# Optimization experiments

Hardware: AMD Instinct MI355X
Metric: run time of the kernel (lower is better)

Reference implementation:

```python
import jax, jax.numpy as jnp
import numpy as np

NT, NP = 100000, 20000
FT, FP, H = 128, 64, 128
E, EL = 2000000, 500000
EPS = 1e-12


def _l2norm(x):
    # F.normalize(x, p=2, dim=-1): x / max(||x||, eps)
    n = jnp.sqrt(jnp.sum(x * x, axis=-1, keepdims=True))
    return x / jnp.maximum(n, EPS)


def _seg_mean(x_src, src_idx, dst_idx, n_dst, inv_cnt):
    # gather src features per edge, scatter-sum to dst, divide by in-degree
    s = jax.ops.segment_sum(x_src[src_idx], dst_idx, num_segments=n_dst)
    return s * inv_cnt[:, None]


def setup_inputs() -> dict:
    key = jax.random.key(0)
    ks = jax.random.split(key, 24)

    def w(k, fan_in, fan_out):
        return jax.random.normal(k, (fan_in, fan_out), jnp.float32) / np.sqrt(fan_in)

    inp = {
        "x_track": jax.random.normal(ks[0], (NT, FT), jnp.float32),
        "x_playlist": jax.random.normal(ks[1], (NP, FP), jnp.float32),
        "edge_src": jax.random.randint(ks[2], (E,), 0, NT),
        "edge_dst": jax.random.randint(ks[3], (E,), 0, NP),
        "label_src": jax.random.randint(ks[4], (EL,), 0, NT),
        "label_dst": jax.random.randint(ks[5], (EL,), 0, NP),
        # per-type input projections (PyG Linear, bias=True)
        "Wn_t": w(ks[6], FT, H), "bn_t": jnp.zeros((H,), jnp.float32),
        "Wn_p": w(ks[7], FP, H), "bn_p": jnp.zeros((H,), jnp.float32),
        # layer1: edge type track->playlist (dst playlist) and reverse (dst track)
        "W1_l_p": w(ks[8], H, H), "b1_p": jnp.zeros((H,), jnp.float32), "W1_r_p": w(ks[9], H, H),
        "W1_l_t": w(ks[10], H, H), "b1_t": jnp.zeros((H,), jnp.float32), "W1_r_t": w(ks[11], H, H),
        # layer2
        "W2_l_p": w(ks[12], H, H), "b2_p": jnp.zeros((H,), jnp.float32), "W2_r_p": w(ks[13], H, H),
        "W2_l_t": w(ks[14], H, H), "b2_t": jnp.zeros((H,), jnp.float32), "W2_r_t": w(ks[15], H, H),
    }
    return inp


def reference(x_track, x_playlist, edge_src, edge_dst, label_src, label_dst,
              Wn_t, bn_t, Wn_p, bn_p,
              W1_l_p, b1_p, W1_r_p, W1_l_t, b1_t, W1_r_t,
              W2_l_p, b2_p, W2_r_p, W2_l_t, b2_t, W2_r_t):
    nt, np_ = x_track.shape[0], x_playlist.shape[0]
    ones = jnp.ones(edge_src.shape, jnp.float32)
    inv_cnt_p = 1.0 / jnp.maximum(jax.ops.segment_sum(ones, edge_dst, num_segments=np_), 1.0)
    inv_cnt_t = 1.0 / jnp.maximum(jax.ops.segment_sum(ones, edge_src, num_segments=nt), 1.0)

    # per-type input linear
    h_t = x_track @ Wn_t + bn_t        # [NT, H]
    h_p = x_playlist @ Wn_p + bn_p     # [NP, H]

    # hetero SAGE layer 1 (normalize=True) + relu
    agg_p = _seg_mean(h_t, edge_src, edge_dst, np_, inv_cnt_p)  # track -> playlist
    agg_t = _seg_mean(h_p, edge_dst, edge_src, nt, inv_cnt_t)   # playlist -> track (rev edges)
    o_p = jax.nn.relu(_l2norm(agg_p @ W1_l_p + b1_p + h_p @ W1_r_p))
    o_t = jax.nn.relu(_l2norm(agg_t @ W1_l_t + b1_t + h_t @ W1_r_t))

    # hetero SAGE layer 2 (normalize=True), no relu
    agg_p2 = _seg_mean(o_t, edge_src, edge_dst, np_, inv_cnt_p)
    agg_t2 = _seg_mean(o_p, edge_dst, edge_src, nt, inv_cnt_t)
    z_p = _l2norm(agg_p2 @ W2_l_p + b2_p + o_p @ W2_r_p)
    z_t = _l2norm(agg_t2 @ W2_l_t + b2_t + o_t @ W2_r_t)

    # link predictor: dot product of endpoint embeddings
    return jnp.sum(z_t[label_src] * z_p[label_dst], axis=-1)  # [EL]
```

## Files before the change

kernel.cpp:

```cpp
#include <hip/hip_runtime.h>
#include <hip/hip_bf16.h>

#define H 128

typedef __attribute__((ext_vector_type(8))) _Float16 f16x8;
typedef __attribute__((ext_vector_type(4))) float f32x4;

static inline size_t align_up(size_t x, size_t a){ return (x + a - 1) & ~(a - 1); }

__device__ inline f32x4 mfma16h(f16x8 a, f16x8 b, f32x4 c){
  return __builtin_amdgcn_mfma_f32_16x16x32_f16(a, b, c, 0, 0, 0);
}

__device__ inline void gload_lds16(const void* g, void* l){
  __builtin_amdgcn_global_load_lds(
      (const __attribute__((address_space(1))) void*)g,
      (__attribute__((address_space(3))) void*)l, 16, 0, 0);
}

struct PackArgs {
  const float* src[10];
  _Float16* dst[10];
  int K[10];
  int start[11];
};

__global__ __launch_bounds__(256) void pack_hist(PackArgs pa, int nblk_pack,
    const int* __restrict__ src, const int* __restrict__ dst, int E,
    int* __restrict__ cnt_b_p, int* __restrict__ cnt_b_t, int histgrid){
  if ((int)blockIdx.x < nblk_pack){
    int t = blockIdx.x * 256 + threadIdx.x;
    if (t >= pa.start[10]) return;
    int m = 0;
    #pragma unroll
    for (int i = 1; i < 10; i++) if (t >= pa.start[i]) m = i;
    int local = t - pa.start[m];
    int k = local >> 7, n = local & 127;
    float w = pa.src[m][local];
    _Float16 hi = (_Float16)w;
    _Float16 lo = (_Float16)(w - (float)hi);
    _Float16* d = pa.dst[m];
    int Km = pa.K[m];
    d[n * Km + k] = hi;
    d[128 * Km + n * Km + k] = lo;
  } else {
    int bid = (int)blockIdx.x - nblk_pack;
    __shared__ int hp[256], ht[256];
    int tid = threadIdx.x;
    hp[tid] = 0; ht[tid] = 0;
    __syncthreads();
    for (int i = bid * 256 + tid; i < E; i += histgrid * 256){
      atomicAdd(&hp[dst[i] >> 7], 1);
      atomicAdd(&ht[src[i] >> 9], 1);
    }
    __syncthreads();
    if (hp[tid]) atomicAdd(&cnt_b_p[tid], hp[tid]);
    if (ht[tid]) atomicAdd(&cnt_b_t[tid], ht[tid]);
  }
}

__global__ void scan_buckets(const int* __restrict__ cb_p, const int* __restrict__ cb_t, int nbp, int nbt,
                             int* __restrict__ base_p, int* __restrict__ base_t,
                             int* __restrict__ cur_p, int* __restrict__ cur_t){
  if (threadIdx.x == 0){
    int s = 0;
    for (int i = 0; i < nbp; i++){ base_p[i] = s; cur_p[i] = s; s += cb_p[i]; }
    base_p[nbp] = s;
  } else if (threadIdx.x == 1){
    int s = 0;
    for (int i = 0; i < nbt; i++){ base_t[i] = s; cur_t[i] = s; s += cb_t[i]; }
    base_t[nbt] = s;
  }
}

__device__ inline void bin_body(const int* __restrict__ keys, const int* __restrict__ vals,
    int E, int shift, int nb, int* __restrict__ cursor, unsigned* __restrict__ rec_out, int chunk,
    int* hist, int* excl, int* gbase, unsigned* recs, unsigned char* binid){
  const int CH = 4096, IT = 16;
  int tid = threadIdx.x;
  int start = chunk * CH;
  int cnt = E - start; if (cnt > CH) cnt = CH;
  if (cnt <= 0) return;
  hist[tid] = 0;
  __syncthreads();
  int b[IT]; int rank[IT]; unsigned rc[IT];
  unsigned mask = (1u << shift) - 1u;
  #pragma unroll
  for (int q = 0; q < IT; q++){
    int i = tid + q * 256;
    if (i < cnt){
      int k = keys[start + i], v = vals[start + i];
      b[q] = k >> shift;
      rc[q] = ((unsigned)v << shift) | ((unsigned)k & mask);
      rank[q] = atomicAdd(&hist[b[q]], 1);
    } else b[q] = -1;
  }
  __syncthreads();
  int lane = tid & 63, wid = tid >> 6;
  if (wid == 0){
    int h0 = hist[lane*4], h1 = hist[lane*4+1], h2 = hist[lane*4+2], h3 = hist[lane*4+3];
    int s = h0 + h1 + h2 + h3;
    int sc = s;
    #pragma unroll
    for (int o = 1; o < 64; o <<= 1){ int t = __shfl_up(sc, (unsigned)o, 64); if (lane >= o) sc += t; }
    int base = sc - s;
    excl[lane*4] = base; excl[lane*4+1] = base + h0;
    excl[lane*4+2] = base + h0 + h1; excl[lane*4+3] = base + h0 + h1 + h2;
  }
  __syncthreads();
  #pragma unroll
  for (int q = 0; q < IT; q++){
    if (b[q] >= 0){
      int pos = excl[b[q]] + rank[q];
      recs[pos] = rc[q];
      binid[pos] = (unsigned char)b[q];
    }
  }
  if (tid < nb && hist[tid] > 0) gbase[tid] = atomicAdd(&cursor[tid], hist[tid]);
  __syncthreads();
  for (int i = tid; i < cnt; i += 256){
    int bb = binid[i];
    rec_out[gbase[bb] + (i - excl[bb])] = recs[i];
  }
}

__global__ __launch_bounds__(256) void bin2(const int* __restrict__ esrc, const int* __restrict__ edst,
    int E, int nb_p, int* cu_p, unsigned* rec_p, int nb_t, int* cu_t, unsigned* rec_t, int nchunks){
  __shared__ int hist[256];
  __shared__ int excl[256];
  __shared__ int gbase[256];
  __shared__ unsigned recs[4096];
  __shared__ unsigned char binid[4096];
  if ((int)blockIdx.x < nchunks)
    bin_body(edst, esrc, E, 7, nb_p, cu_p, rec_p, blockIdx.x, hist, excl, gbase, recs, binid);
  else
    bin_body(esrc, edst, E, 9, nb_t, cu_t, rec_t, blockIdx.x - nchunks, hist, excl, gbase, recs, binid);
}

template<int LOC, int LB>
__device__ inline void build_body(const unsigned* __restrict__ rec, const int* __restrict__ bbase,
    int nkeys, int E, int* __restrict__ off, float* __restrict__ inv, int* __restrict__ csr,
    int b, int nb, int* hist, int* excl, int* cur, int* wsum){
  int tid = threadIdx.x;
  int s = bbase[b], e = bbase[b + 1];
  for (int k = tid; k < LOC; k += 256){ hist[k] = 0; cur[k] = 0; }
  __syncthreads();
  for (int i = s + tid; i < e; i += 256) atomicAdd(&hist[rec[i] & (LOC - 1)], 1);
  __syncthreads();
  int lane = tid & 63, wid = tid >> 6;
  constexpr int BPT = (LOC + 255) / 256;
  int h[BPT]; int ssum = 0;
  #pragma unroll
  for (int q = 0; q < BPT; q++){
    int k = tid * BPT + q;
    h[q] = (k < LOC) ? hist[k] : 0;
    ssum += h[q];
  }
  int sc = ssum;
  #pragma unroll
  for (int o = 1; o < 64; o <<= 1){ int t = __shfl_up(sc, (unsigned)o, 64); if (lane >= o) sc += t; }
  if (lane == 63) wsum[wid] = sc;
  __syncthreads();
  int base = 0;
  for (int w = 0; w < wid; w++) base += wsum[w];
  int ex = base + sc - ssum;
  #pragma unroll
  for (int q = 0; q < BPT; q++){
    int k = tid * BPT + q;
    if (k < LOC) excl[k] = ex;
    ex += h[q];
  }
  __syncthreads();
  int keybase = b << LB;
  for (int k = tid; k < LOC; k += 256){
    int gk = keybase + k;
    if (gk < nkeys){
      off[gk] = s + excl[k];
      int c = hist[k];
      inv[gk] = 1.0f / (float)(c > 1 ? c : 1);
    }
  }
  if (b == nb - 1 && tid == 0) off[nkeys] = E;
  for (int i = s + tid; i < e; i += 256){
    unsigned r = rec[i];
    int k = (int)(r & (LOC - 1));
    int rk = atomicAdd(&cur[k], 1);
    csr[s + excl[k] + rk] = (int)(r >> LB);
  }
}

__global__ __launch_bounds__(256) void build2(
    const unsigned* rec_p, const int* bb_p, int NPk, int* off_p, float* inv_p, int* csr_p, int nb_p,
    const unsigned* rec_t, const int* bb_t, int NTk, int* off_t, float* inv_t, int* csr_t, int nb_t, int E){
  __shared__ int hist[512];
  __shared__ int excl[512];
  __shared__ int cur[512];
  __shared__ int wsum[8];
  if ((int)blockIdx.x < nb_p)
    build_body<128,7>(rec_p, bb_p, NPk, E, off_p, inv_p, csr_p, blockIdx.x, nb_p, hist, excl, cur, wsum);
  else
    build_body<512,9>(rec_t, bb_t, NTk, E, off_t, inv_t, csr_t, blockIdx.x - nb_p, nb_t, hist, excl, cur, wsum);
}

struct ProjJob {
  const float* A;
  const _Float16* WT;
  const float* bias;
  _Float16* OUT;
  int M;
  int ntiles;
  int nblk;
};
template<int KA>
__device__ inline void proj_body(ProjJob j, int bid, char* lds){
  constexpr int KST = KA / 32;
  constexpr int RB_A = KA * 4;
  constexpr int CHA = RB_A / 16;
  constexpr int NIA = 64 * CHA / 512;
  constexpr int ABYTES = 64 * RB_A;

  const int t    = threadIdx.x;
  const int wid  = t >> 6;
  const int lane = t & 63;
  const int l15  = lane & 15;
  const int lkg  = lane >> 4;
  const int colg = wid * 16 + l15;
  const int M = j.M, ntiles = j.ntiles, nblk = j.nblk;

  f16x8 wl_hi[KST], wl_lo[KST];
  {
    const _Float16* bh = j.WT + (size_t)colg * KA + lkg * 8;
    #pragma unroll
    for (int ks = 0; ks < KST; ks++){
      wl_hi[ks] = *(const f16x8*)(bh + ks * 32);
      wl_lo[ks] = *(const f16x8*)(bh + 128 * KA + ks * 32);
    }
  }
  const float bb = j.bias[colg];

  auto stage = [&](int tile, char* dstA){
    int row0 = tile * 64;
    #pragma unroll
    for (int q = 0; q < NIA; q++){
      int lc  = q * 512 + t;
      int row = lc / CHA;
      int ch  = lc - row * CHA;
      int grow = row0 + row; if (grow > M - 1) grow = M - 1;
      int gch = ch ^ (row & 7);
      gload_lds16((const char*)j.A + (size_t)grow * RB_A + gch * 16, dstA + lc * 16);
    }
  };

  int p = 0;
  if (bid < ntiles) stage(bid, lds);

  for (int t0 = bid; t0 < ntiles; t0 += nblk){
    const int row0 = t0 * 64;
    const int tn = t0 + nblk;
    const bool hasnext = tn < ntiles;
    if (hasnext) stage(tn, lds + (p ^ 1) * ABYTES);

    if (hasnext){
      if constexpr (NIA == 4) asm volatile("s_waitcnt vmcnt(4)" ::: "memory");
      else                    asm volatile("s_waitcnt vmcnt(2)" ::: "memory");
    } else {
      asm volatile("s_waitcnt vmcnt(0)" ::: "memory");
    }
    __builtin_amdgcn_s_barrier();
    asm volatile("" ::: "memory");

    const char* bufA = lds + p * ABYTES;

    f32x4 acc[4];
    #pragma unroll
    for (int tt = 0; tt < 4; tt++){
      acc[tt] = (f32x4){0.f, 0.f, 0.f, 0.f};
      const int rl = tt * 16 + l15;
      const int sw = rl & 7;
      const char* ap = bufA + rl * RB_A;
      #pragma unroll
      for (int ks = 0; ks < KST; ks++){
        int c0 = lkg * 2 + ks * 8;
        f32x4 a0 = *(const f32x4*)(ap + ((c0    ) ^ sw) * 16);
        f32x4 a1 = *(const f32x4*)(ap + ((c0 + 1) ^ sw) * 16);
        f16x8 af;
        #pragma unroll
        for (int e = 0; e < 8; e++) af[e] = (_Float16)(e < 4 ? a0[e] : a1[e - 4]);
        acc[tt] = mfma16h(af, wl_hi[ks], acc[tt]);
        acc[tt] = mfma16h(af, wl_lo[ks], acc[tt]);
      }
      acc[tt].x += bb; acc[tt].y += bb; acc[tt].z += bb; acc[tt].w += bb;
    }

    #pragma unroll
    for (int tt = 0; tt < 4; tt++){
      #pragma unroll
      for (int r = 0; r < 4; r++){
        int row = row0 + tt * 16 + lkg * 4 + r;
        if (row < M) j.OUT[(size_t)row * H + colg] = (_Float16)acc[tt][r];
      }
    }
    asm volatile("s_waitcnt lgkmcnt(0)" ::: "memory");
    __builtin_amdgcn_s_barrier();
    asm volatile("" ::: "memory");
    p ^= 1;
  }
}
__global__ __launch_bounds__(512) void proj2(ProjJob jt, ProjJob jp){
  __shared__ __align__(16) char lds[2 * 64 * 512];
  if ((int)blockIdx.x < jt.nblk) proj_body<128>(jt, blockIdx.x, lds);
  else                           proj_body<64>(jp, (int)blockIdx.x - jt.nblk, lds);
}

struct SageJob {
  const _Float16* A;
  const _Float16* Bs;
  const _Float16* WlT;
  const _Float16* WrT;
  const float* bias;
  _Float16* OUT;
  int M;
  int ntiles;
  int nblk;
};
template<bool RELU>
__global__ __launch_bounds__(512) void sage_mfma2(SageJob j0, SageJob j1){
  constexpr int KST = 4;
  constexpr int CHA = 16;
  constexpr int NIA = 2, NIB = 2;
  constexpr int ABYTES = 64 * 256;
  constexpr int BUFB = 2 * ABYTES;

  __shared__ __align__(16) char lds[2 * BUFB];
  __shared__ float red[8][64];

  const bool second = (int)blockIdx.x >= j0.nblk;
  const SageJob j = second ? j1 : j0;
  const int bid = (int)blockIdx.x - (second ? j0.nblk : 0);
  const int M = j.M, ntiles = j.ntiles, nblk = j.nblk;

  const int t    = threadIdx.x;
  const int wid  = t >> 6;
  const int lane = t & 63;
  const int l15  = lane & 15;
  const int lkg  = lane >> 4;
  const int colg = wid * 16 + l15;

  f16x8 wl_hi[KST], wl_lo[KST], wr_hi[KST], wr_lo[KST];
  {
    const _Float16* bh = j.WlT + (size_t)colg * 128 + lkg * 8;
    const _Float16* bh2 = j.WrT + (size_t)colg * 128 + lkg * 8;
    #pragma unroll
    for (int ks = 0; ks < KST; ks++){
      wl_hi[ks] = *(const f16x8*)(bh + ks * 32);
      wl_lo[ks] = *(const f16x8*)(bh + 128 * 128 + ks * 32);
      wr_hi[ks] = *(const f16x8*)(bh2 + ks * 32);
      wr_lo[ks] = *(const f16x8*)(bh2 + 128 * 128 + ks * 32);
    }
  }
  const float bb = j.bias[colg];

  auto stage = [&](int tile, char* dstA, char* dstB){
    int row0 = tile * 64;
    #pragma unroll
    for (int q = 0; q < NIA; q++){
      int lc  = q * 512 + t;
      int row = lc / CHA;
      int ch  = lc - row * CHA;
      int grow = row0 + row; if (grow > M - 1) grow = M - 1;
      int gch = ch ^ (row & 7);
      gload_lds16((const char*)j.A + (size_t)grow * 256 + gch * 16, dstA + lc * 16);
    }
    #pragma unroll
    for (int q = 0; q < NIB; q++){
      int lc  = q * 512 + t;
      int row = lc >> 4;
      int ch  = lc & 15;
      int grow = row0 + row; if (grow > M - 1) grow = M - 1;
      int gch = ch ^ (row & 7);
      gload_lds16((const char*)j.Bs + (size_t)grow * 256 + gch * 16, dstB + lc * 16);
    }
  };

  int p = 0;
  if (bid < ntiles) stage(bid, lds, lds + ABYTES);

  for (int t0 = bid; t0 < ntiles; t0 += nblk){
    const int row0 = t0 * 64;
    const int tn = t0 + nblk;
    const bool hasnext = tn < ntiles;
    if (hasnext) stage(tn, lds + (p ^ 1) * BUFB, lds + (p ^ 1) * BUFB + ABYTES);

    if (hasnext) asm volatile("s_waitcnt vmcnt(4)" ::: "memory");
    else         asm volatile("s_waitcnt vmcnt(0)" ::: "memory");
    __builtin_amdgcn_s_barrier();
    asm volatile("" ::: "memory");

    const char* bufA = lds + p * BUFB;
    const char* bufB = bufA + ABYTES;

    f32x4 acc[4];
    #pragma unroll
    for (int tt = 0; tt < 4; tt++){
      acc[tt] = (f32x4){0.f, 0.f, 0.f, 0.f};
      const int rl = tt * 16 + l15;
      const int sw = rl & 7;
      const char* ap = bufA + rl * 256;
      #pragma unroll
      for (int ks = 0; ks < KST; ks++){
        f16x8 af = *(const f16x8*)(ap + ((ks * 4 + lkg) ^ sw) * 16);
        acc[tt] = mfma16h(af, wl_hi[ks], acc[tt]);
        acc[tt] = mfma16h(af, wl_lo[ks], acc[tt]);
      }
      const char* bp = bufB + rl * 256;
      #pragma unroll
      for (int ks = 0; ks < KST; ks++){
        f16x8 bf = *(const f16x8*)(bp + ((ks * 4 + lkg) ^ sw) * 16);
        acc[tt] = mfma16h(bf, wr_hi[ks], acc[tt]);
        acc[tt] = mfma16h(bf, wr_lo[ks], acc[tt]);
      }
      acc[tt].x += bb; acc[tt].y += bb; acc[tt].z += bb; acc[tt].w += bb;
    }

    #pragma unroll
    for (int tt = 0; tt < 4; tt++){
      #pragma unroll
      for (int r = 0; r < 4; r++){
        float v = acc[tt][r] * acc[tt][r];
        v += __shfl_xor(v, 1, 64);
        v += __shfl_xor(v, 2, 64);
        v += __shfl_xor(v, 4, 64);
        v += __shfl_xor(v, 8, 64);
        if (l15 == 0) red[wid][tt * 16 + lkg * 4 + r] = v;
      }
    }
    asm volatile("s_waitcnt lgkmcnt(0)" ::: "memory");
    __builtin_amdgcn_s_barrier();
    asm volatile("" ::: "memory");
    #pragma unroll
    for (int tt = 0; tt < 4; tt++){
      #pragma unroll
      for (int r = 0; r < 4; r++){
        int idx = tt * 16 + lkg * 4 + r;
        float s = 0.f;
        #pragma unroll
        for (int w2 = 0; w2 < 8; w2++) s += red[w2][idx];
        float scale = 1.f / fmaxf(sqrtf(s), 1e-12f);
        float v = acc[tt][r] * scale;
        if (RELU) v = fmaxf(v, 0.f);
        acc[tt][r] = v;
      }
    }
    #pragma unroll
    for (int tt = 0; tt < 4; tt++){
      #pragma unroll
      for (int r = 0; r < 4; r++){
        int row = row0 + tt * 16 + lkg * 4 + r;
        if (row < M) j.OUT[(size_t)row * H + colg] = (_Float16)acc[tt][r];
      }
    }
    p ^= 1;
  }
}

struct AggJob {
  const _Float16* feat;
  const int* csr;
  const int* off;
  const float* inv;
  _Float16* out;
  int n;
  int nblk;
};
__global__ __launch_bounds__(256) void agg2_kernel(AggJob j0, AggJob j1){
  const bool second = (int)blockIdx.x >= j0.nblk;
  const AggJob j = second ? j1 : j0;
  const int bid = (int)blockIdx.x - (second ? j0.nblk : 0);
  int g = bid * 16 + (threadIdx.x >> 4);
  int l = threadIdx.x & 15;
  if (g >= j.n) return;
  int s = j.off[g], e = j.off[g + 1];
  float c0[8], c1[8], c2[8], c3[8];
  #pragma unroll
  for (int q = 0; q < 8; q++){ c0[q] = 0.f; c1[q] = 0.f; c2[q] = 0.f; c3[q] = 0.f; }
  const _Float16* F = j.feat;
  int i = s;
  for (; i + 3 < e; i += 4){
    f16x8 v0 = *(const f16x8*)(F + (size_t)j.csr[i]     * H + l * 8);
    f16x8 v1 = *(const f16x8*)(F + (size_t)j.csr[i + 1] * H + l * 8);
    f16x8 v2 = *(const f16x8*)(F + (size_t)j.csr[i + 2] * H + l * 8);
    f16x8 v3 = *(const f16x8*)(F + (size_t)j.csr[i + 3] * H + l * 8);
    #pragma unroll
    for (int q = 0; q < 8; q++){
      c0[q] += (float)v0[q]; c1[q] += (float)v1[q];
      c2[q] += (float)v2[q]; c3[q] += (float)v3[q];
    }
  }
  for (; i < e; i++){
    f16x8 v0 = *(const f16x8*)(F + (size_t)j.csr[i] * H + l * 8);
    #pragma unroll
    for (int q = 0; q < 8; q++) c0[q] += (float)v0[q];
  }
  float iv = j.inv[g];
  f16x8 ov;
  #pragma unroll
  for (int q = 0; q < 8; q++){
    float r = (c0[q] + c1[q]) + (c2[q] + c3[q]);
    ov[q] = (_Float16)(r * iv);
  }
  *(f16x8*)(j.out + (size_t)g * H + l * 8) = ov;
}

__global__ __launch_bounds__(256) void dot_kernel(const _Float16* __restrict__ zt, const _Float16* __restrict__ zp,
                           const int* __restrict__ ls, const int* __restrict__ ld,
                           float* __restrict__ out, int n){
  int w = (blockIdx.x * 256 + threadIdx.x) >> 4;
  int l = threadIdx.x & 15;
  if (w >= n) return;
  f16x8 x = *(const f16x8*)&zt[(size_t)ls[w] * H + l * 8];
  f16x8 y = *(const f16x8*)&zp[(size_t)ld[w] * H + l * 8];
  float v = 0.f;
  #pragma unroll
  for (int q = 0; q < 8; q++) v += (float)x[q] * (float)y[q];
  v += __shfl_xor(v, 1, 64);
  v += __shfl_xor(v, 2, 64);
  v += __shfl_xor(v, 4, 64);
  v += __shfl_xor(v, 8, 64);
  if (l == 0) out[w] = v;
}

extern "C" void kernel_launch(void* const* d_in, const int* in_sizes, int n_in,
                              void* d_out, int out_size, void* d_ws, size_t ws_size,
                              hipStream_t stream){
  const float* x_t  = (const float*)d_in[0];
  const float* x_p  = (const float*)d_in[1];
  const int*   esrc = (const int*)d_in[2];
  const int*   edst = (const int*)d_in[3];
  const int*   lsrc = (const int*)d_in[4];
  const int*   ldst = (const int*)d_in[5];
  const float* Wn_t = (const float*)d_in[6];
  const float* bn_t = (const float*)d_in[7];
  const float* Wn_p = (const float*)d_in[8];
  const float* bn_p = (const float*)d_in[9];
  const float* W1_l_p=(const float*)d_in[10]; const float* b1_p=(const float*)d_in[11]; const float* W1_r_p=(const float*)d_in[12];
  const float* W1_l_t=(const float*)d_in[13]; const float* b1_t=(const float*)d_in[14]; const float* W1_r_t=(const float*)d_in[15];
  const float* W2_l_p=(const float*)d_in[16]; const float* b2_p=(const float*)d_in[17]; const float* W2_r_p=(const float*)d_in[18];
  const float* W2_l_t=(const float*)d_in[19]; const float* b2_t=(const float*)d_in[20]; const float* W2_r_t=(const float*)d_in[21];
  float* out = (float*)d_out;

  const int FT = 128, FP = 64;
  int NT = in_sizes[0] / FT;
  int NP = in_sizes[1] / FP;
  int E  = in_sizes[2];
  int EL = in_sizes[4];

  const int SH_P = 7, SH_T = 9;
  int nb_p = (NP + (1 << SH_P) - 1) >> SH_P;
  int nb_t = (NT + (1 << SH_T) - 1) >> SH_T;

  char* base = (char*)d_ws;
  size_t o = 0;
  auto alloc = [&](size_t bytes) -> char* { char* p = base + o; o = align_up(o + bytes, 256); return p; };
  int*   cb_p  = (int*)alloc(256 * 4);
  int*   cb_t  = (int*)alloc(256 * 4);
  size_t zero_bytes = o;
  int*   bb_p  = (int*)alloc(260 * 4);
  int*   bb_t  = (int*)alloc(260 * 4);
  int*   cu_p  = (int*)alloc(256 * 4);
  int*   cu_t  = (int*)alloc(256 * 4);
  int*   off_p = (int*)alloc((size_t)(NP + 1) * 4);
  int*   off_t = (int*)alloc((size_t)(NT + 1) * 4);
  float* inv_p = (float*)alloc((size_t)NP * 4);
  float* inv_t = (float*)alloc((size_t)NT * 4);
  unsigned* rec_p = (unsigned*)alloc((size_t)E * 4);
  unsigned* rec_t = (unsigned*)alloc((size_t)E * 4);
  int*   csr_p = (int*)alloc((size_t)E * 4);
  int*   csr_t = (int*)alloc((size_t)E * 4);
  _Float16* h_t = (_Float16*)alloc((size_t)NT * H * 2);
  _Float16* h_p = (_Float16*)alloc((size_t)NP * H * 2);
  _Float16* a_t = (_Float16*)alloc((size_t)NT * H * 2);
  _Float16* a_p = (_Float16*)alloc((size_t)NP * H * 2);

  PackArgs pa;
  const float* wsrc[10] = {Wn_t, Wn_p, W1_l_p, W1_r_p, W1_l_t, W1_r_t, W2_l_p, W2_r_p, W2_l_t, W2_r_t};
  int Ks[10] = {128, 64, 128, 128, 128, 128, 128, 128, 128, 128};
  _Float16* wpk[10];
  int st = 0;
  for (int m = 0; m < 10; m++){
    wpk[m] = (_Float16*)alloc((size_t)2 * 128 * Ks[m] * 2);
    pa.src[m] = wsrc[m]; pa.dst[m] = wpk[m]; pa.K[m] = Ks[m]; pa.start[m] = st;
    st += Ks[m] * 128;
  }
  pa.start[10] = st;
  (void)ws_size; (void)n_in; (void)out_size;

  hipMemsetAsync(base, 0, zero_bytes, stream);

  int nblk_pack = (st + 255) / 256;
  const int histgrid = 512;
  pack_hist<<<nblk_pack + histgrid, 256, 0, stream>>>(pa, nblk_pack, esrc, edst, E, cb_p, cb_t, histgrid);
  scan_buckets<<<1, 64, 0, stream>>>(cb_p, cb_t, nb_p, nb_t, bb_p, bb_t, cu_p, cu_t);
  int nchunks = (E + 4095) / 4096;
  bin2<<<2 * nchunks, 256, 0, stream>>>(esrc, edst, E, nb_p, cu_p, rec_p, nb_t, cu_t, rec_t, nchunks);
  build2<<<nb_p + nb_t, 256, 0, stream>>>(rec_p, bb_p, NP, off_p, inv_p, csr_p, nb_p,
                                          rec_t, bb_t, NT, off_t, inv_t, csr_t, nb_t, E);

  int tiles_t = (NT + 63) / 64;
  int tiles_p = (NP + 63) / 64;
  int pblk_t = tiles_t < 448 ? tiles_t : 448;
  int pblk_p = tiles_p < 64 ? tiles_p : 64;
  ProjJob pjt{x_t, wpk[0], bn_t, h_t, NT, tiles_t, pblk_t};
  ProjJob pjp{x_p, wpk[1], bn_p, h_p, NP, tiles_p, pblk_p};
  proj2<<<pblk_t + pblk_p, 512, 0, stream>>>(pjt, pjp);

  int ablk_p = (NP + 15) / 16;
  int ablk_t = (NT + 15) / 16;
  AggJob aj_p1{h_t, csr_p, off_p, inv_p, a_p, NP, ablk_p};
  AggJob aj_t1{h_p, csr_t, off_t, inv_t, a_t, NT, ablk_t};
  AggJob aj_p2{a_t, csr_p, off_p, inv_p, h_p, NP, ablk_p};
  AggJob aj_t2{a_p, csr_t, off_t, inv_t, h_t, NT, ablk_t};

  int nblk_p = tiles_p < 96 ? tiles_p : 96;
  int nblk_t = tiles_t < 416 ? tiles_t : 416;
  SageJob sj1p{a_p, h_p, wpk[2], wpk[3], b1_p, a_p, NP, tiles_p, nblk_p};
  SageJob sj1t{a_t, h_t, wpk[4], wpk[5], b1_t, a_t, NT, tiles_t, nblk_t};
  SageJob sj2p{h_p, a_p, wpk[6], wpk[7], b2_p, h_p, NP, tiles_p, nblk_p};
  SageJob sj2t{h_t, a_t, wpk[8], wpk[9], b2_t, h_t, NT, tiles_t, nblk_t};

  agg2_kernel<<<ablk_p + ablk_t, 256, 0, stream>>>(aj_p1, aj_t1);
  sage_mfma2<true><<<nblk_p + nblk_t, 512, 0, stream>>>(sj1p, sj1t);

  agg2_kernel<<<ablk_p + ablk_t, 256, 0, stream>>>(aj_p2, aj_t2);
  sage_mfma2<false><<<nblk_p + nblk_t, 512, 0, stream>>>(sj2p, sj2t);

  dot_kernel<<<(EL + 15) / 16, 256, 0, stream>>>(h_t, h_p, lsrc, ldst, out, EL);
}
```

Baseline: 505.8 us.

## Fuse neighbor mean aggregation into SAGE MFMA kernel via LDS tile

The separate gather-mean aggregation kernel is folded into the SAGE linear kernel. Each 512-thread block now gathers and averages neighbor features for its own 64-row tile and writes them straight into a swizzled LDS buffer, while the self features are loaded asynchronously into LDS. It then runs the MFMA, L2-normalisation and activation epilogue. This removes the round trip of the aggregated features through global memory and two kernel launches per forward pass. In exchange it drops the persistent double-buffered tile loop, launches one block per tile, and reloads the weight fragments in every block.

```diff
diff --git a/kernel.cpp b/kernel.cpp
--- a/kernel.cpp
+++ b/kernel.cpp
@@ -312,8 +312,11 @@
   else                           proj_body<64>(jp, (int)blockIdx.x - jt.nblk, lds);
 }
 
-struct SageJob {
-  const _Float16* A;
+struct FusedJob {
+  const _Float16* feat;
+  const int* csr;
+  const int* off;
+  const float* inv;
   const _Float16* Bs;
   const _Float16* WlT;
   const _Float16* WrT;
@@ -321,23 +324,18 @@
   _Float16* OUT;
   int M;
   int ntiles;
-  int nblk;
 };
 template<bool RELU>
-__global__ __launch_bounds__(512) void sage_mfma2(SageJob j0, SageJob j1){
-  constexpr int KST = 4;
-  constexpr int CHA = 16;
-  constexpr int NIA = 2, NIB = 2;
-  constexpr int ABYTES = 64 * 256;
-  constexpr int BUFB = 2 * ABYTES;
-
-  __shared__ __align__(16) char lds[2 * BUFB];
+__global__ __launch_bounds__(512) void fused_sage(FusedJob j0, FusedJob j1){
+  __shared__ __align__(16) char ldsA[64 * 256];
+  __shared__ __align__(16) char ldsB[64 * 256];
   __shared__ float red[8][64];
 
-  const bool second = (int)blockIdx.x >= j0.nblk;
-  const SageJob j = second ? j1 : j0;
-  const int bid = (int)blockIdx.x - (second ? j0.nblk : 0);
-  const int M = j.M, ntiles = j.ntiles, nblk = j.nblk;
+  const bool second = (int)blockIdx.x >= j0.ntiles;
+  const FusedJob j = second ? j1 : j0;
+  const int tile = (int)blockIdx.x - (second ? j0.ntiles : 0);
+  const int M = j.M;
+  const int row0 = tile * 64;
 
   const int t    = threadIdx.x;
   const int wid  = t >> 6;
@@ -346,12 +344,61 @@
   const int lkg  = lane >> 4;
   const int colg = wid * 16 + l15;
 
-  f16x8 wl_hi[KST], wl_lo[KST], wr_hi[KST], wr_lo[KST];
+  #pragma unroll
+  for (int q = 0; q < 2; q++){
+    int lc = q * 512 + t;
+    int row = lc >> 4, ch = lc & 15;
+    int grow = row0 + row; if (grow > M - 1) grow = M - 1;
+    int gch = ch ^ (row & 7);
+    gload_lds16((const char*)j.Bs + (size_t)grow * 256 + gch * 16, ldsB + lc * 16);
+  }
+
   {
-    const _Float16* bh = j.WlT + (size_t)colg * 128 + lkg * 8;
+    const int g = t >> 4, l = t & 15;
+    const _Float16* F = j.feat;
+    #pragma unroll
+    for (int rr = 0; rr < 2; rr++){
+      int r  = g * 2 + rr;
+      int gr = row0 + r;
+      int grc = gr < M ? gr : M - 1;
+      int s = j.off[grc], e = j.off[grc + 1];
+      float c0[8], c1[8], c2[8], c3[8];
+      #pragma unroll
+      for (int q = 0; q < 8; q++){ c0[q] = 0.f; c1[q] = 0.f; c2[q] = 0.f; c3[q] = 0.f; }
+      int i = s;
+      for (; i + 3 < e; i += 4){
+        f16x8 v0 = *(const f16x8*)(F + (size_t)j.csr[i]     * H + l * 8);
+        f16x8 v1 = *(const f16x8*)(F + (size_t)j.csr[i + 1] * H + l * 8);
+        f16x8 v2 = *(const f16x8*)(F + (size_t)j.csr[i + 2] * H + l * 8);
+        f16x8 v3 = *(const f16x8*)(F + (size_t)j.csr[i + 3] * H + l * 8);
+        #pragma unroll
+        for (int q = 0; q < 8; q++){
+          c0[q] += (float)v0[q]; c1[q] += (float)v1[q];
+          c2[q] += (float)v2[q]; c3[q] += (float)v3[q];
+        }
+      }
+      for (; i < e; i++){
+        f16x8 v0 = *(const f16x8*)(F + (size_t)j.csr[i] * H + l * 8);
+        #pragma unroll
+        for (int q = 0; q < 8; q++) c0[q] += (float)v0[q];
+      }
+      float iv = j.inv[grc];
+      f16x8 ov;
+      #pragma unroll
+      for (int q = 0; q < 8; q++){
+        float rv = (c0[q] + c1[q]) + (c2[q] + c3[q]);
+        ov[q] = (_Float16)(rv * iv);
+      }
+      *(f16x8*)(ldsA + r * 256 + ((l ^ (r & 7)) * 16)) = ov;
+    }
+  }
+
+  f16x8 wl_hi[4], wl_lo[4], wr_hi[4], wr_lo[4];
+  {
+    const _Float16* bh  = j.WlT + (size_t)colg * 128 + lkg * 8;
     const _Float16* bh2 = j.WrT + (size_t)colg * 128 + lkg * 8;
     #pragma unroll
-    for (int ks = 0; ks < KST; ks++){
+    for (int ks = 0; ks < 4; ks++){
       wl_hi[ks] = *(const f16x8*)(bh + ks * 32);
       wl_lo[ks] = *(const f16x8*)(bh + 128 * 128 + ks * 32);
       wr_hi[ks] = *(const f16x8*)(bh2 + ks * 32);
@@ -360,155 +407,70 @@
   }
   const float bb = j.bias[colg];
 
-  auto stage = [&](int tile, char* dstA, char* dstB){
-    int row0 = tile * 64;
-    #pragma unroll
-    for (int q = 0; q < NIA; q++){
-      int lc  = q * 512 + t;
-      int row = lc / CHA;
-      int ch  = lc - row * CHA;
-      int grow = row0 + row; if (grow > M - 1) grow = M - 1;
-      int gch = ch ^ (row & 7);
-      gload_lds16((const char*)j.A + (size_t)grow * 256 + gch * 16, dstA + lc * 16);
-    }
-    #pragma unroll
-    for (int q = 0; q < NIB; q++){
-      int lc  = q * 512 + t;
-      int row = lc >> 4;
-      int ch  = lc & 15;
-      int grow = row0 + row; if (grow > M - 1) grow = M - 1;
-      int gch = ch ^ (row & 7);
-      gload_lds16((const char*)j.Bs + (size_t)grow * 256 + gch * 16, dstB + lc * 16);
-    }
-  };
-
-  int p = 0;
-  if (bid < ntiles) stage(bid, lds, lds + ABYTES);
-
-  for (int t0 = bid; t0 < ntiles; t0 += nblk){
-    const int row0 = t0 * 64;
-    const int tn = t0 + nblk;
-    const bool hasnext = tn < ntiles;
-    if (hasnext) stage(tn, lds + (p ^ 1) * BUFB, lds + (p ^ 1) * BUFB + ABYTES);
-
-    if (hasnext) asm volatile("s_waitcnt vmcnt(4)" ::: "memory");
-    else         asm volatile("s_waitcnt vmcnt(0)" ::: "memory");
-    __builtin_amdgcn_s_barrier();
-    asm volatile("" ::: "memory");
-
-    const char* bufA = lds + p * BUFB;
-    const char* bufB = bufA + ABYTES;
-
-    f32x4 acc[4];
-    #pragma unroll
-    for (int tt = 0; tt < 4; tt++){
-      acc[tt] = (f32x4){0.f, 0.f, 0.f, 0.f};
-      const int rl = tt * 16 + l15;
-      const int sw = rl & 7;
-      const char* ap = bufA + rl * 256;
+  asm volatile("s_waitcnt vmcnt(0) lgkmcnt(0)" ::: "memory");
+  __builtin_amdgcn_s_barrier();
+  asm volatile("" ::: "memory");
+
+  f32x4 acc[4];
+  #pragma unroll
+  for (int tt = 0; tt < 4; tt++){
+    acc[tt] = (f32x4){0.f, 0.f, 0.f, 0.f};
+    const int rl = tt * 16 + l15;
+    const int sw = rl & 7;
+    const char* ap = ldsA + rl * 256;
+    #pragma unroll
+    for (int ks = 0; ks < 4; ks++){
+      f16x8 af = *(const f16x8*)(ap + ((ks * 4 + lkg) ^ sw) * 16);
+      acc[tt] = mfma16h(af, wl_hi[ks], acc[tt]);
+      acc[tt] = mfma16h(af, wl_lo[ks], acc[tt]);
+    }
+    const char* bp = ldsB + rl * 256;
+    #pragma unroll
+    for (int ks = 0; ks < 4; ks++){
+      f16x8 bf = *(const f16x8*)(bp + ((ks * 4 + lkg) ^ sw) * 16);
+      acc[tt] = mfma16h(bf, wr_hi[ks], acc[tt]);
+      acc[tt] = mfma16h(bf, wr_lo[ks], acc[tt]);
+    }
+    acc[tt].x += bb; acc[tt].y += bb; acc[tt].z += bb; acc[tt].w += bb;
+  }
+
+  #pragma unroll
+  for (int tt = 0; tt < 4; tt++){
+    #pragma unroll
+    for (int r = 0; r < 4; r++){
+      float v = acc[tt][r] * acc[tt][r];
+      v += __shfl_xor(v, 1, 64);
+      v += __shfl_xor(v, 2, 64);
+      v += __shfl_xor(v, 4, 64);
+      v += __shfl_xor(v, 8, 64);
+      if (l15 == 0) red[wid][tt * 16 + lkg * 4 + r] = v;
+    }
+  }
+  asm volatile("s_waitcnt lgkmcnt(0)" ::: "memory");
+  __builtin_amdgcn_s_barrier();
+  asm volatile("" ::: "memory");
+  #pragma unroll
+  for (int tt = 0; tt < 4; tt++){
+    #pragma unroll
+    for (int r = 0; r < 4; r++){
+      int idx = tt * 16 + lkg * 4 + r;
+      float s = 0.f;
       #pragma unroll
-      for (int ks = 0; ks < KST; ks++){
-        f16x8 af = *(const f16x8*)(ap + ((ks * 4 + lkg) ^ sw) * 16);
-        acc[tt] = mfma16h(af, wl_hi[ks], acc[tt]);
-        acc[tt] = mfma16h(af, wl_lo[ks], acc[tt]);
-      }
-      const char* bp = bufB + rl * 256;
-      #pragma unroll
-      for (int ks = 0; ks < KST; ks++){
-        f16x8 bf = *(const f16x8*)(bp + ((ks * 4 + lkg) ^ sw) * 16);
-        acc[tt] = mfma16h(bf, wr_hi[ks], acc[tt]);
-        acc[tt] = mfma16h(bf, wr_lo[ks], acc[tt]);
-      }
-      acc[tt].x += bb; acc[tt].y += bb; acc[tt].z += bb; acc[tt].w += bb;
-    }
-
-    #pragma unroll
-    for (int tt = 0; tt < 4; tt++){
-      #pragma unroll
-      for (int r = 0; r < 4; r++){
-        float v = acc[tt][r] * acc[tt][r];
-        v += __shfl_xor(v, 1, 64);
-        v += __shfl_xor(v, 2, 64);
-        v += __shfl_xor(v, 4, 64);
-        v += __shfl_xor(v, 8, 64);
-        if (l15 == 0) red[wid][tt * 16 + lkg * 4 + r] = v;
-      }
-    }
-    asm volatile("s_waitcnt lgkmcnt(0)" ::: "memory");
-    __builtin_amdgcn_s_barrier();
-    asm volatile("" ::: "memory");
-    #pragma unroll
-    for (int tt = 0; tt < 4; tt++){
-      #pragma unroll
-      for (int r = 0; r < 4; r++){
-        int idx = tt * 16 + lkg * 4 + r;
-        float s = 0.f;
-        #pragma unroll
-        for (int w2 = 0; w2 < 8; w2++) s += red[w2][idx];
-        float scale = 1.f / fmaxf(sqrtf(s), 1e-12f);
-        float v = acc[tt][r] * scale;
-        if (RELU) v = fmaxf(v, 0.f);
-        acc[tt][r] = v;
-      }
-    }
-    #pragma unroll
-    for (int tt = 0; tt < 4; tt++){
-      #pragma unroll
-      for (int r = 0; r < 4; r++){
-        int row = row0 + tt * 16 + lkg * 4 + r;
-        if (row < M) j.OUT[(size_t)row * H + colg] = (_Float16)acc[tt][r];
-      }
-    }
-    p ^= 1;
-  }
-}
-
-struct AggJob {
-  const _Float16* feat;
-  const int* csr;
-  const int* off;
-  const float* inv;
-  _Float16* out;
-  int n;
-  int nblk;
-};
-__global__ __launch_bounds__(256) void agg2_kernel(AggJob j0, AggJob j1){
-  const bool second = (int)blockIdx.x >= j0.nblk;
-  const AggJob j = second ? j1 : j0;
-  const int bid = (int)blockIdx.x - (second ? j0.nblk : 0);
-  int g = bid * 16 + (threadIdx.x >> 4);
-  int l = threadIdx.x & 15;
-  if (g >= j.n) return;
-  int s = j.off[g], e = j.off[g + 1];
-  float c0[8], c1[8], c2[8], c3[8];
-  #pragma unroll
-  for (int q = 0; q < 8; q++){ c0[q] = 0.f; c1[q] = 0.f; c2[q] = 0.f; c3[q] = 0.f; }
-  const _Float16* F = j.feat;
-  int i = s;
-  for (; i + 3 < e; i += 4){
-    f16x8 v0 = *(const f16x8*)(F + (size_t)j.csr[i]     * H + l * 8);
-    f16x8 v1 = *(const f16x8*)(F + (size_t)j.csr[i + 1] * H + l * 8);
-    f16x8 v2 = *(const f16x8*)(F + (size_t)j.csr[i + 2] * H + l * 8);
-    f16x8 v3 = *(const f16x8*)(F + (size_t)j.csr[i + 3] * H + l * 8);
-    #pragma unroll
-    for (int q = 0; q < 8; q++){
-      c0[q] += (float)v0[q]; c1[q] += (float)v1[q];
-      c2[q] += (float)v2[q]; c3[q] += (float)v3[q];
-    }
-  }
-  for (; i < e; i++){
-    f16x8 v0 = *(const f16x8*)(F + (size_t)j.csr[i] * H + l * 8);
-    #pragma unroll
-    for (int q = 0; q < 8; q++) c0[q] += (float)v0[q];
-  }
-  float iv = j.inv[g];
-  f16x8 ov;
-  #pragma unroll
-  for (int q = 0; q < 8; q++){
-    float r = (c0[q] + c1[q]) + (c2[q] + c3[q]);
-    ov[q] = (_Float16)(r * iv);
-  }
-  *(f16x8*)(j.out + (size_t)g * H + l * 8) = ov;
+      for (int w2 = 0; w2 < 8; w2++) s += red[w2][idx];
+      float scale = 1.f / fmaxf(sqrtf(s), 1e-12f);
+      float v = acc[tt][r] * scale;
+      if (RELU) v = fmaxf(v, 0.f);
+      acc[tt][r] = v;
+    }
+  }
+  #pragma unroll
+  for (int tt = 0; tt < 4; tt++){
+    #pragma unroll
+    for (int r = 0; r < 4; r++){
+      int row = row0 + tt * 16 + lkg * 4 + r;
+      if (row < M) j.OUT[(size_t)row * H + colg] = (_Float16)acc[tt][r];
+    }
+  }
 }
 
 __global__ __launch_bounds__(256) void dot_kernel(const _Float16* __restrict__ zt, const _Float16* __restrict__ zp,
@@ -613,25 +575,13 @@
   ProjJob pjp{x_p, wpk[1], bn_p, h_p, NP, tiles_p, pblk_p};
   proj2<<<pblk_t + pblk_p, 512, 0, stream>>>(pjt, pjp);
 
-  int ablk_p = (NP + 15) / 16;
-  int ablk_t = (NT + 15) / 16;
-  AggJob aj_p1{h_t, csr_p, off_p, inv_p, a_p, NP, ablk_p};
-  AggJob aj_t1{h_p, csr_t, off_t, inv_t, a_t, NT, ablk_t};
-  AggJob aj_p2{a_t, csr_p, off_p, inv_p, h_p, NP, ablk_p};
-  AggJob aj_t2{a_p, csr_t, off_t, inv_t, h_t, NT, ablk_t};
-
-  int nblk_p = tiles_p < 96 ? tiles_p : 96;
-  int nblk_t = tiles_t < 416 ? tiles_t : 416;
-  SageJob sj1p{a_p, h_p, wpk[2], wpk[3], b1_p, a_p, NP, tiles_p, nblk_p};
-  SageJob sj1t{a_t, h_t, wpk[4], wpk[5], b1_t, a_t, NT, tiles_t, nblk_t};
-  SageJob sj2p{h_p, a_p, wpk[6], wpk[7], b2_p, h_p, NP, tiles_p, nblk_p};
-  SageJob sj2t{h_t, a_t, wpk[8], wpk[9], b2_t, h_t, NT, tiles_t, nblk_t};
-
-  agg2_kernel<<<ablk_p + ablk_t, 256, 0, stream>>>(aj_p1, aj_t1);
-  sage_mfma2<true><<<nblk_p + nblk_t, 512, 0, stream>>>(sj1p, sj1t);
-
-  agg2_kernel<<<ablk_p + ablk_t, 256, 0, stream>>>(aj_p2, aj_t2);
-  sage_mfma2<false><<<nblk_p + nblk_t, 512, 0, stream>>>(sj2p, sj2t);
+  FusedJob f1p{h_t, csr_p, off_p, inv_p, h_p, wpk[2], wpk[3], b1_p, a_p, NP, tiles_p};
+  FusedJob f1t{h_p, csr_t, off_t, inv_t, h_t, wpk[4], wpk[5], b1_t, a_t, NT, tiles_t};
+  fused_sage<true><<<tiles_p + tiles_t, 512, 0, stream>>>(f1p, f1t);
+
+  FusedJob f2p{a_t, csr_p, off_p, inv_p, a_p, wpk[6], wpk[7], b2_p, h_p, NP, tiles_p};
+  FusedJob f2t{a_p, csr_t, off_t, inv_t, a_t, wpk[8], wpk[9], b2_t, h_t, NT, tiles_t};
+  fused_sage<false><<<tiles_p + tiles_t, 512, 0, stream>>>(f2p, f2t);
 
   dot_kernel<<<(EL + 15) / 16, 256, 0, stream>>>(h_t, h_p, lsrc, ldst, out, EL);
 }
```

After: 643.1 us. +27.1%, slower.
